# Performance work log

Hardware: AMD Instinct MI355X
Metric: run time of the kernel (lower is better)

Reference implementation:

```python
import jax, jax.numpy as jnp
import numpy as np

EMBED_DIM = 512
N_HEADS = 8
HEAD_DIM = EMBED_DIM // N_HEADS


def setup_inputs() -> dict:
    key = jax.random.key(0)
    ks = jax.random.split(key, 8)
    B, S, D = 8, 2048, EMBED_DIM
    scale = 1.0 / np.sqrt(D)
    return {
        "key": jax.random.normal(ks[0], (B, S, D), dtype=jnp.float32),
        "query": jax.random.normal(ks[1], (B, S, D), dtype=jnp.float32),
        "value": jax.random.normal(ks[2], (B, S, D), dtype=jnp.float32),
        # nn.Linear stores weight as [out, in]; y = x @ W.T. We store W_T=[in,out].
        "Wq": jax.random.normal(ks[3], (D, D), dtype=jnp.float32) * scale,
        "Wk": jax.random.normal(ks[4], (D, D), dtype=jnp.float32) * scale,
        "Wv": jax.random.normal(ks[5], (D, D), dtype=jnp.float32) * scale,
        "Wo": jax.random.normal(ks[6], (D, D), dtype=jnp.float32) * scale,
        "bo": jax.random.normal(ks[7], (D,), dtype=jnp.float32) * scale,
    }


def reference(key, query, value, Wq, Wk, Wv, Wo, bo):
    B, S, D = key.shape
    Sq = query.shape[1]
    H, Hd = N_HEADS, HEAD_DIM
    # projections (no bias for q/k/v)
    q = (query @ Wq).reshape(B, Sq, H, Hd)
    k = (key @ Wk).reshape(B, S, H, Hd)
    v = (value @ Wv).reshape(B, S, H, Hd)
    # scores: [B, H, Sq, S]
    product = jnp.einsum("bqhd,bkhd->bhqk", q, k) / np.sqrt(Hd)
    scores = jax.nn.softmax(product, axis=-1)
    out = jnp.einsum("bhqk,bkhd->bqhd", scores, v).reshape(B, Sq, D)
    return out @ Wo + bo
```

## Files before the change

### kernel.cpp

```cpp
#include <hip/hip_runtime.h>

typedef _Float16 half8 __attribute__((ext_vector_type(8)));
typedef _Float16 half4 __attribute__((ext_vector_type(4)));
typedef float floatx16 __attribute__((ext_vector_type(16)));

#define MFMA_F16 __builtin_amdgcn_mfma_f32_32x32x16_f16

__device__ __forceinline__ half8 ld_frag_lds(const _Float16* p) {
    union { half8 v; half4 h[2]; } u;
    u.h[0] = *(const half4*)(p);
    u.h[1] = *(const half4*)(p + 4);
    return u.v;
}

__global__ __launch_bounds__(256) void wcvt_kernel(const float* __restrict__ Wq,
                                                   const float* __restrict__ Wk,
                                                   const float* __restrict__ Wv,
                                                   const float* __restrict__ Wo,
                                                   _Float16* __restrict__ Wt) {
    int idx = blockIdx.x * 256 + threadIdx.x;
    int wsel = idx >> 18;
    int rem  = idx & 262143;
    int o = rem >> 9;
    int i = rem & 511;
    const float* src = (wsel == 0) ? Wq : (wsel == 1) ? Wk : (wsel == 2) ? Wv : Wo;
    Wt[idx] = (_Float16)src[i * 512 + o];
}

template <int MODE>
__global__ __launch_bounds__(256, 3) void gemm_kernel(const void* __restrict__ Aptr,
                                                      const _Float16* __restrict__ Wt,
                                                      const float* __restrict__ bias,
                                                      void* __restrict__ outp,
                                                      float oscale) {
    __shared__ _Float16 Alds[128 * 68];
    __shared__ _Float16 Blds[128 * 68];

    const int tid  = threadIdx.x;
    const int lane = tid & 63;
    const int w    = tid >> 6;
    const int l31  = lane & 31;
    const int lh   = lane >> 5;
    const int wm   = w >> 1;
    const int wn   = w & 1;
    const int n0   = blockIdx.x * 128;
    const int m0   = blockIdx.y * 128;

    const int crow = tid >> 3;
    const int ck8  = (tid & 7) * 8;

    floatx16 acc[2][2];
#pragma unroll
    for (int i = 0; i < 2; i++)
#pragma unroll
        for (int j = 0; j < 2; j++)
#pragma unroll
            for (int r = 0; r < 16; r++) acc[i][j][r] = 0.0f;

    float4 apre_f[4][2];
    int4   apre_h[4];
    if (MODE == 2) {
        const _Float16* Ah = (const _Float16*)Aptr;
#pragma unroll
        for (int i = 0; i < 4; i++)
            apre_h[i] = *(const int4*)(Ah + (size_t)(m0 + crow + 32 * i) * 512 + ck8);
    } else {
        const float* Af = (const float*)Aptr;
#pragma unroll
        for (int i = 0; i < 4; i++) {
            const float* p = Af + (size_t)(m0 + crow + 32 * i) * 512 + ck8;
            apre_f[i][0] = *(const float4*)(p);
            apre_f[i][1] = *(const float4*)(p + 4);
        }
    }

    for (int t = 0; t < 8; t++) {
        const int ks = t * 64;
        int4 bpre[4];
#pragma unroll
        for (int i = 0; i < 4; i++)
            bpre[i] = *(const int4*)(Wt + (size_t)(n0 + crow + 32 * i) * 512 + ks + ck8);

        __syncthreads();
#pragma unroll
        for (int i = 0; i < 4; i++) {
            int r = crow + 32 * i;
            if (MODE == 2) {
                *(int2*)&Alds[r * 68 + ck8]     = make_int2(apre_h[i].x, apre_h[i].y);
                *(int2*)&Alds[r * 68 + ck8 + 4] = make_int2(apre_h[i].z, apre_h[i].w);
            } else {
                float4 f0 = apre_f[i][0], f1 = apre_f[i][1];
                half4 h0 = {(_Float16)f0.x, (_Float16)f0.y, (_Float16)f0.z, (_Float16)f0.w};
                half4 h1 = {(_Float16)f1.x, (_Float16)f1.y, (_Float16)f1.z, (_Float16)f1.w};
                *(half4*)&Alds[r * 68 + ck8]     = h0;
                *(half4*)&Alds[r * 68 + ck8 + 4] = h1;
            }
            *(int2*)&Blds[r * 68 + ck8]     = make_int2(bpre[i].x, bpre[i].y);
            *(int2*)&Blds[r * 68 + ck8 + 4] = make_int2(bpre[i].z, bpre[i].w);
        }
        __syncthreads();

        if (t < 7) {
            if (MODE == 2) {
                const _Float16* Ah = (const _Float16*)Aptr;
#pragma unroll
                for (int i = 0; i < 4; i++)
                    apre_h[i] = *(const int4*)(Ah + (size_t)(m0 + crow + 32 * i) * 512 + ks + 64 + ck8);
            } else {
                const float* Af = (const float*)Aptr;
#pragma unroll
                for (int i = 0; i < 4; i++) {
                    const float* p = Af + (size_t)(m0 + crow + 32 * i) * 512 + ks + 64 + ck8;
                    apre_f[i][0] = *(const float4*)(p);
                    apre_f[i][1] = *(const float4*)(p + 4);
                }
            }
        }

#pragma unroll
        for (int kc = 0; kc < 4; kc++) {
            int kb = kc * 16 + lh * 8;
            half8 af[2], bf[2];
            af[0] = ld_frag_lds(&Alds[(wm * 64 + l31) * 68 + kb]);
            af[1] = ld_frag_lds(&Alds[(wm * 64 + 32 + l31) * 68 + kb]);
            bf[0] = ld_frag_lds(&Blds[(wn * 64 + l31) * 68 + kb]);
            bf[1] = ld_frag_lds(&Blds[(wn * 64 + 32 + l31) * 68 + kb]);
#pragma unroll
            for (int i = 0; i < 2; i++)
#pragma unroll
                for (int j = 0; j < 2; j++)
                    acc[i][j] = MFMA_F16(af[i], bf[j], acc[i][j], 0, 0, 0);
        }
    }

#pragma unroll
    for (int i = 0; i < 2; i++) {
#pragma unroll
        for (int j = 0; j < 2; j++) {
            int gn    = n0 + wn * 64 + j * 32 + l31;
            int mbase = m0 + wm * 64 + i * 32 + 4 * lh;
            if (MODE == 0) {
                _Float16* out = (_Float16*)outp;
                int h = gn >> 6, hd = gn & 63;
#pragma unroll
                for (int r = 0; r < 16; r++) {
                    int gm = mbase + (r & 3) + 8 * (r >> 2);
                    int b = gm >> 11, s = gm & 2047;
                    out[(size_t)((b * 8 + h) * 2048 + s) * 64 + hd] =
                        (_Float16)(acc[i][j][r] * oscale);
                }
            } else if (MODE == 1) {
                _Float16* out = (_Float16*)outp;
                int h = gn >> 6, hd = gn & 63;
#pragma unroll
                for (int g = 0; g < 4; g++) {
                    int gm = mbase + 8 * g;
                    int b = gm >> 11, s = gm & 2047;
                    half4 pk = {(_Float16)acc[i][j][4 * g + 0], (_Float16)acc[i][j][4 * g + 1],
                                (_Float16)acc[i][j][4 * g + 2], (_Float16)acc[i][j][4 * g + 3]};
                    *(half4*)&out[(size_t)((b * 8 + h) * 64 + hd) * 2048 + s] = pk;
                }
            } else {
                float* out = (float*)outp;
                float bv = bias[gn];
#pragma unroll
                for (int r = 0; r < 16; r++) {
                    int gm = mbase + (r & 3) + 8 * (r >> 2);
                    out[(size_t)gm * 512 + gn] = acc[i][j][r] + bv;
                }
            }
        }
    }
}

__global__ __launch_bounds__(256, 4) void attn_kernel(const _Float16* __restrict__ Qg,
                                                      const _Float16* __restrict__ Kg,
                                                      const _Float16* __restrict__ Vg,
                                                      _Float16* __restrict__ AO) {
    __shared__ _Float16 Klds[64 * 68];
    __shared__ _Float16 Vlds[64 * 68];
    __shared__ _Float16 Plds[4][32 * 68];

    const int tid  = threadIdx.x;
    const int lane = tid & 63;
    const int w    = tid >> 6;
    const int l31  = lane & 31;
    const int lh   = lane >> 5;
    const int h    = blockIdx.y;
    const int b    = blockIdx.z;
    const int q0   = blockIdx.x * 128 + w * 32;

    const size_t bhoff = (size_t)(b * 8 + h) * (2048 * 64);
    const _Float16* Qbh = Qg + bhoff;
    const _Float16* Kbh = Kg + bhoff;
    const _Float16* Vbh = Vg + bhoff;

    half8 qf[4];
#pragma unroll
    for (int kc = 0; kc < 4; kc++)
        qf[kc] = *(const half8*)(Qbh + (size_t)(q0 + l31) * 64 + kc * 16 + lh * 8);

    floatx16 O[2];
#pragma unroll
    for (int i = 0; i < 2; i++)
#pragma unroll
        for (int r = 0; r < 16; r++) O[i][r] = 0.0f;
    float lsum = 0.0f;

    for (int kt = 0; kt < 32; kt++) {
        __syncthreads();
        {
            const _Float16* Ksrc = Kbh + (size_t)kt * (64 * 64);
            const _Float16* Vsrc = Vbh + (size_t)kt * 64;
#pragma unroll
            for (int i = 0; i < 2; i++) {
                int c = tid + 256 * i;
                int row = c >> 3, k8 = (c & 7) * 8;
                int4 dk = *(const int4*)(Ksrc + row * 64 + k8);
                *(int2*)&Klds[row * 68 + k8]     = make_int2(dk.x, dk.y);
                *(int2*)&Klds[row * 68 + k8 + 4] = make_int2(dk.z, dk.w);
                int4 dv = *(const int4*)(Vsrc + (size_t)row * 2048 + k8);
                *(int2*)&Vlds[row * 68 + k8]     = make_int2(dv.x, dv.y);
                *(int2*)&Vlds[row * 68 + k8 + 4] = make_int2(dv.z, dv.w);
            }
        }
        __syncthreads();

        floatx16 Sf[2];
#pragma unroll
        for (int i = 0; i < 2; i++)
#pragma unroll
            for (int r = 0; r < 16; r++) Sf[i][r] = 0.0f;
#pragma unroll
        for (int ms = 0; ms < 2; ms++)
#pragma unroll
            for (int kc = 0; kc < 4; kc++) {
                half8 kf = ld_frag_lds(&Klds[(ms * 32 + l31) * 68 + kc * 16 + lh * 8]);
                Sf[ms] = MFMA_F16(kf, qf[kc], Sf[ms], 0, 0, 0);
            }

        float rsum = 0.0f;
#pragma unroll
        for (int ms = 0; ms < 2; ms++) {
#pragma unroll
            for (int g = 0; g < 4; g++) {
                float p0 = exp2f(Sf[ms][4 * g + 0]);
                float p1 = exp2f(Sf[ms][4 * g + 1]);
                float p2 = exp2f(Sf[ms][4 * g + 2]);
                float p3 = exp2f(Sf[ms][4 * g + 3]);
                rsum += (p0 + p1) + (p2 + p3);
                half4 pk = {(_Float16)p0, (_Float16)p1, (_Float16)p2, (_Float16)p3};
                *(half4*)&Plds[w][l31 * 68 + ms * 32 + g * 8 + lh * 4] = pk;
            }
        }
        lsum += rsum;

#pragma unroll
        for (int kc = 0; kc < 4; kc++) {
            half8 pf = ld_frag_lds(&Plds[w][l31 * 68 + kc * 16 + lh * 8]);
#pragma unroll
            for (int hs = 0; hs < 2; hs++) {
                half8 vf = ld_frag_lds(&Vlds[(hs * 32 + l31) * 68 + kc * 16 + lh * 8]);
                O[hs] = MFMA_F16(vf, pf, O[hs], 0, 0, 0);
            }
        }
    }

    lsum += __shfl_xor(lsum, 32);
    float inv = 1.0f / lsum;
    int q = q0 + l31;
#pragma unroll
    for (int hs = 0; hs < 2; hs++) {
#pragma unroll
        for (int g = 0; g < 4; g++) {
            half4 pk = {(_Float16)(O[hs][4 * g + 0] * inv),
                        (_Float16)(O[hs][4 * g + 1] * inv),
                        (_Float16)(O[hs][4 * g + 2] * inv),
                        (_Float16)(O[hs][4 * g + 3] * inv)};
            *(half4*)&AO[(size_t)(b * 2048 + q) * 512 + h * 64 + hs * 32 + g * 8 + lh * 4] = pk;
        }
    }
}

extern "C" void kernel_launch(void* const* d_in, const int* in_sizes, int n_in,
                              void* d_out, int out_size, void* d_ws, size_t ws_size,
                              hipStream_t stream) {
    const float* key   = (const float*)d_in[0];
    const float* query = (const float*)d_in[1];
    const float* value = (const float*)d_in[2];
    const float* Wq    = (const float*)d_in[3];
    const float* Wk    = (const float*)d_in[4];
    const float* Wv    = (const float*)d_in[5];
    const float* Wo    = (const float*)d_in[6];
    const float* bo    = (const float*)d_in[7];

    _Float16* ws = (_Float16*)d_ws;
    _Float16* Wt = ws;
    _Float16* Qh = ws + 1048576;
    _Float16* Kh = Qh + 8388608;
    _Float16* Vt = Kh + 8388608;
    _Float16* AO = Vt + 8388608;

    const float C1 = 0.18033688011112042f;

    wcvt_kernel<<<dim3(4096), dim3(256), 0, stream>>>(Wq, Wk, Wv, Wo, Wt);

    gemm_kernel<0><<<dim3(4, 128), dim3(256), 0, stream>>>(query, Wt,            nullptr, Qh, C1);
    gemm_kernel<0><<<dim3(4, 128), dim3(256), 0, stream>>>(key,   Wt + 262144,   nullptr, Kh, 1.0f);
    gemm_kernel<1><<<dim3(4, 128), dim3(256), 0, stream>>>(value, Wt + 2*262144, nullptr, Vt, 1.0f);

    attn_kernel<<<dim3(16, 8, 8), dim3(256), 0, stream>>>(Qh, Kh, Vt, AO);

    gemm_kernel<2><<<dim3(4, 128), dim3(256), 0, stream>>>(AO, Wt + 3*262144, bo, (float*)d_out, 1.0f);
}
```

Measured before the change: 334.5 us.

## Merge QKV GEMMs, prefetch K/V tiles in attention, tile weight transpose

Merges the three projection GEMM launches into one 3D grid, which removes launch gaps and leaves the GPU less idle at kernel tails. The weight conversion becomes an LDS-tiled transpose, so global reads and writes are coalesced. The attention kernel now register-prefetches the next K/V tile so the global loads overlap the MFMA work, and the GEMM B loads are double-buffered the same way. It also uses a hardware exp2 and packed round-toward-zero fp16 conversions, which raise register pressure and change rounding slightly.

Measured after the change: 298.1 us. -10.9%, faster.

```diff
diff --git a/kernel.cpp b/kernel.cpp
--- a/kernel.cpp
+++ b/kernel.cpp
@@ -2,9 +2,25 @@
 
 typedef _Float16 half8 __attribute__((ext_vector_type(8)));
 typedef _Float16 half4 __attribute__((ext_vector_type(4)));
+typedef __fp16 fp16x2 __attribute__((ext_vector_type(2)));
 typedef float floatx16 __attribute__((ext_vector_type(16)));
 
 #define MFMA_F16 __builtin_amdgcn_mfma_f32_32x32x16_f16
+
+__device__ __forceinline__ float fast_exp2(float x) {
+#if __has_builtin(__builtin_amdgcn_exp2f)
+    return __builtin_amdgcn_exp2f(x);
+#else
+    return exp2f(x);
+#endif
+}
+
+__device__ __forceinline__ half4 pack4(float a, float b, float c, float d) {
+    union { fp16x2 p[2]; half4 h; } u;
+    u.p[0] = __builtin_amdgcn_cvt_pkrtz(a, b);
+    u.p[1] = __builtin_amdgcn_cvt_pkrtz(c, d);
+    return u.h;
+}
 
 __device__ __forceinline__ half8 ld_frag_lds(const _Float16* p) {
     union { half8 v; half4 h[2]; } u;
@@ -18,23 +34,52 @@
                                                    const float* __restrict__ Wv,
                                                    const float* __restrict__ Wo,
                                                    _Float16* __restrict__ Wt) {
-    int idx = blockIdx.x * 256 + threadIdx.x;
-    int wsel = idx >> 18;
-    int rem  = idx & 262143;
-    int o = rem >> 9;
-    int i = rem & 511;
+    __shared__ _Float16 T[64 * 68];
+    const int bx   = blockIdx.x;
+    const int wsel = bx >> 6;
+    const int tile = bx & 63;
+    const int to   = (tile >> 3) * 64;
+    const int ti   = (tile & 7) * 64;
     const float* src = (wsel == 0) ? Wq : (wsel == 1) ? Wk : (wsel == 2) ? Wv : Wo;
-    Wt[idx] = (_Float16)src[i * 512 + o];
-}
-
-template <int MODE>
-__global__ __launch_bounds__(256, 3) void gemm_kernel(const void* __restrict__ Aptr,
-                                                      const _Float16* __restrict__ Wt,
-                                                      const float* __restrict__ bias,
-                                                      void* __restrict__ outp,
-                                                      float oscale) {
+    const int t = threadIdx.x;
+    const int rloc = t >> 4, c4 = (t & 15) * 4;
+#pragma unroll
+    for (int m = 0; m < 4; m++) {
+        int i = ti + rloc + 16 * m;
+        float4 f = *(const float4*)(src + (size_t)i * 512 + to + c4);
+        T[(c4 + 0) * 68 + rloc + 16 * m] = (_Float16)f.x;
+        T[(c4 + 1) * 68 + rloc + 16 * m] = (_Float16)f.y;
+        T[(c4 + 2) * 68 + rloc + 16 * m] = (_Float16)f.z;
+        T[(c4 + 3) * 68 + rloc + 16 * m] = (_Float16)f.w;
+    }
+    __syncthreads();
+    const int o_loc = t >> 2, ich = (t & 3) * 16;
+    const _Float16* s = &T[o_loc * 68 + ich];
+    _Float16* dst = Wt + (size_t)wsel * 262144 + (size_t)(to + o_loc) * 512 + ti + ich;
+    half4 a0 = *(const half4*)(s);
+    half4 a1 = *(const half4*)(s + 4);
+    half4 a2 = *(const half4*)(s + 8);
+    half4 a3 = *(const half4*)(s + 12);
+    *(half4*)(dst)      = a0;
+    *(half4*)(dst + 4)  = a1;
+    *(half4*)(dst + 8)  = a2;
+    *(half4*)(dst + 12) = a3;
+}
+
+__global__ __launch_bounds__(256, 3) void qkv_gemm(const float* __restrict__ query,
+                                                   const float* __restrict__ key,
+                                                   const float* __restrict__ value,
+                                                   const _Float16* __restrict__ Wt,
+                                                   _Float16* __restrict__ Qh,
+                                                   _Float16* __restrict__ Kh,
+                                                   _Float16* __restrict__ Vt,
+                                                   float C1) {
     __shared__ _Float16 Alds[128 * 68];
     __shared__ _Float16 Blds[128 * 68];
+
+    const int z = blockIdx.z;
+    const float* A = (z == 0) ? query : (z == 1) ? key : value;
+    const _Float16* W = Wt + (size_t)z * 262144;
 
     const int tid  = threadIdx.x;
     const int lane = tid & 63;
@@ -45,7 +90,6 @@
     const int wn   = w & 1;
     const int n0   = blockIdx.x * 128;
     const int m0   = blockIdx.y * 128;
-
     const int crow = tid >> 3;
     const int ck8  = (tid & 7) * 8;
 
@@ -57,66 +101,38 @@
 #pragma unroll
             for (int r = 0; r < 16; r++) acc[i][j][r] = 0.0f;
 
-    float4 apre_f[4][2];
-    int4   apre_h[4];
-    if (MODE == 2) {
-        const _Float16* Ah = (const _Float16*)Aptr;
-#pragma unroll
-        for (int i = 0; i < 4; i++)
-            apre_h[i] = *(const int4*)(Ah + (size_t)(m0 + crow + 32 * i) * 512 + ck8);
-    } else {
-        const float* Af = (const float*)Aptr;
-#pragma unroll
-        for (int i = 0; i < 4; i++) {
-            const float* p = Af + (size_t)(m0 + crow + 32 * i) * 512 + ck8;
-            apre_f[i][0] = *(const float4*)(p);
-            apre_f[i][1] = *(const float4*)(p + 4);
-        }
+    float4 apre[4][2];
+    int4   bpre[4];
+#pragma unroll
+    for (int i = 0; i < 4; i++) {
+        const float* p = A + (size_t)(m0 + crow + 32 * i) * 512 + ck8;
+        apre[i][0] = *(const float4*)(p);
+        apre[i][1] = *(const float4*)(p + 4);
+        bpre[i] = *(const int4*)(W + (size_t)(n0 + crow + 32 * i) * 512 + ck8);
     }
 
     for (int t = 0; t < 8; t++) {
-        const int ks = t * 64;
-        int4 bpre[4];
-#pragma unroll
-        for (int i = 0; i < 4; i++)
-            bpre[i] = *(const int4*)(Wt + (size_t)(n0 + crow + 32 * i) * 512 + ks + ck8);
-
         __syncthreads();
 #pragma unroll
         for (int i = 0; i < 4; i++) {
             int r = crow + 32 * i;
-            if (MODE == 2) {
-                *(int2*)&Alds[r * 68 + ck8]     = make_int2(apre_h[i].x, apre_h[i].y);
-                *(int2*)&Alds[r * 68 + ck8 + 4] = make_int2(apre_h[i].z, apre_h[i].w);
-            } else {
-                float4 f0 = apre_f[i][0], f1 = apre_f[i][1];
-                half4 h0 = {(_Float16)f0.x, (_Float16)f0.y, (_Float16)f0.z, (_Float16)f0.w};
-                half4 h1 = {(_Float16)f1.x, (_Float16)f1.y, (_Float16)f1.z, (_Float16)f1.w};
-                *(half4*)&Alds[r * 68 + ck8]     = h0;
-                *(half4*)&Alds[r * 68 + ck8 + 4] = h1;
-            }
-            *(int2*)&Blds[r * 68 + ck8]     = make_int2(bpre[i].x, bpre[i].y);
-            *(int2*)&Blds[r * 68 + ck8 + 4] = make_int2(bpre[i].z, bpre[i].w);
-        }
-        __syncthreads();
-
+            float4 f0 = apre[i][0], f1 = apre[i][1];
+            *(half4*)&Alds[r * 68 + ck8]     = pack4(f0.x, f0.y, f0.z, f0.w);
+            *(half4*)&Alds[r * 68 + ck8 + 4] = pack4(f1.x, f1.y, f1.z, f1.w);
+            *(int2*)&Blds[r * 68 + ck8]      = make_int2(bpre[i].x, bpre[i].y);
+            *(int2*)&Blds[r * 68 + ck8 + 4]  = make_int2(bpre[i].z, bpre[i].w);
+        }
+        __syncthreads();
         if (t < 7) {
-            if (MODE == 2) {
-                const _Float16* Ah = (const _Float16*)Aptr;
-#pragma unroll
-                for (int i = 0; i < 4; i++)
-                    apre_h[i] = *(const int4*)(Ah + (size_t)(m0 + crow + 32 * i) * 512 + ks + 64 + ck8);
-            } else {
-                const float* Af = (const float*)Aptr;
-#pragma unroll
-                for (int i = 0; i < 4; i++) {
-                    const float* p = Af + (size_t)(m0 + crow + 32 * i) * 512 + ks + 64 + ck8;
-                    apre_f[i][0] = *(const float4*)(p);
-                    apre_f[i][1] = *(const float4*)(p + 4);
-                }
-            }
-        }
-
+            int ks2 = (t + 1) * 64;
+#pragma unroll
+            for (int i = 0; i < 4; i++) {
+                const float* p = A + (size_t)(m0 + crow + 32 * i) * 512 + ks2 + ck8;
+                apre[i][0] = *(const float4*)(p);
+                apre[i][1] = *(const float4*)(p + 4);
+                bpre[i] = *(const int4*)(W + (size_t)(n0 + crow + 32 * i) * 512 + ks2 + ck8);
+            }
+        }
 #pragma unroll
         for (int kc = 0; kc < 4; kc++) {
             int kb = kc * 16 + lh * 8;
@@ -133,41 +149,117 @@
         }
     }
 
+    const float oscale = (z == 0) ? C1 : 1.0f;
+    _Float16* out01 = (z == 0) ? Qh : Kh;
 #pragma unroll
     for (int i = 0; i < 2; i++) {
 #pragma unroll
         for (int j = 0; j < 2; j++) {
             int gn    = n0 + wn * 64 + j * 32 + l31;
             int mbase = m0 + wm * 64 + i * 32 + 4 * lh;
-            if (MODE == 0) {
-                _Float16* out = (_Float16*)outp;
-                int h = gn >> 6, hd = gn & 63;
+            int h = gn >> 6, hd = gn & 63;
+            if (z < 2) {
 #pragma unroll
                 for (int r = 0; r < 16; r++) {
                     int gm = mbase + (r & 3) + 8 * (r >> 2);
                     int b = gm >> 11, s = gm & 2047;
-                    out[(size_t)((b * 8 + h) * 2048 + s) * 64 + hd] =
+                    out01[(size_t)((b * 8 + h) * 2048 + s) * 64 + hd] =
                         (_Float16)(acc[i][j][r] * oscale);
                 }
-            } else if (MODE == 1) {
-                _Float16* out = (_Float16*)outp;
-                int h = gn >> 6, hd = gn & 63;
+            } else {
 #pragma unroll
                 for (int g = 0; g < 4; g++) {
                     int gm = mbase + 8 * g;
                     int b = gm >> 11, s = gm & 2047;
-                    half4 pk = {(_Float16)acc[i][j][4 * g + 0], (_Float16)acc[i][j][4 * g + 1],
-                                (_Float16)acc[i][j][4 * g + 2], (_Float16)acc[i][j][4 * g + 3]};
-                    *(half4*)&out[(size_t)((b * 8 + h) * 64 + hd) * 2048 + s] = pk;
+                    *(half4*)&Vt[(size_t)((b * 8 + h) * 64 + hd) * 2048 + s] =
+                        pack4(acc[i][j][4 * g + 0], acc[i][j][4 * g + 1],
+                              acc[i][j][4 * g + 2], acc[i][j][4 * g + 3]);
                 }
-            } else {
-                float* out = (float*)outp;
-                float bv = bias[gn];
-#pragma unroll
-                for (int r = 0; r < 16; r++) {
-                    int gm = mbase + (r & 3) + 8 * (r >> 2);
-                    out[(size_t)gm * 512 + gn] = acc[i][j][r] + bv;
-                }
+            }
+        }
+    }
+}
+
+__global__ __launch_bounds__(256, 3) void out_gemm(const _Float16* __restrict__ A,
+                                                   const _Float16* __restrict__ W,
+                                                   const float* __restrict__ bias,
+                                                   float* __restrict__ out) {
+    __shared__ _Float16 Alds[128 * 68];
+    __shared__ _Float16 Blds[128 * 68];
+
+    const int tid  = threadIdx.x;
+    const int lane = tid & 63;
+    const int w    = tid >> 6;
+    const int l31  = lane & 31;
+    const int lh   = lane >> 5;
+    const int wm   = w >> 1;
+    const int wn   = w & 1;
+    const int n0   = blockIdx.x * 128;
+    const int m0   = blockIdx.y * 128;
+    const int crow = tid >> 3;
+    const int ck8  = (tid & 7) * 8;
+
+    floatx16 acc[2][2];
+#pragma unroll
+    for (int i = 0; i < 2; i++)
+#pragma unroll
+        for (int j = 0; j < 2; j++)
+#pragma unroll
+            for (int r = 0; r < 16; r++) acc[i][j][r] = 0.0f;
+
+    int4 apre[4], bpre[4];
+#pragma unroll
+    for (int i = 0; i < 4; i++) {
+        apre[i] = *(const int4*)(A + (size_t)(m0 + crow + 32 * i) * 512 + ck8);
+        bpre[i] = *(const int4*)(W + (size_t)(n0 + crow + 32 * i) * 512 + ck8);
+    }
+
+    for (int t = 0; t < 8; t++) {
+        __syncthreads();
+#pragma unroll
+        for (int i = 0; i < 4; i++) {
+            int r = crow + 32 * i;
+            *(int2*)&Alds[r * 68 + ck8]     = make_int2(apre[i].x, apre[i].y);
+            *(int2*)&Alds[r * 68 + ck8 + 4] = make_int2(apre[i].z, apre[i].w);
+            *(int2*)&Blds[r * 68 + ck8]     = make_int2(bpre[i].x, bpre[i].y);
+            *(int2*)&Blds[r * 68 + ck8 + 4] = make_int2(bpre[i].z, bpre[i].w);
+        }
+        __syncthreads();
+        if (t < 7) {
+            int ks2 = (t + 1) * 64;
+#pragma unroll
+            for (int i = 0; i < 4; i++) {
+                apre[i] = *(const int4*)(A + (size_t)(m0 + crow + 32 * i) * 512 + ks2 + ck8);
+                bpre[i] = *(const int4*)(W + (size_t)(n0 + crow + 32 * i) * 512 + ks2 + ck8);
+            }
+        }
+#pragma unroll
+        for (int kc = 0; kc < 4; kc++) {
+            int kb = kc * 16 + lh * 8;
+            half8 af[2], bf[2];
+            af[0] = ld_frag_lds(&Alds[(wm * 64 + l31) * 68 + kb]);
+            af[1] = ld_frag_lds(&Alds[(wm * 64 + 32 + l31) * 68 + kb]);
+            bf[0] = ld_frag_lds(&Blds[(wn * 64 + l31) * 68 + kb]);
+            bf[1] = ld_frag_lds(&Blds[(wn * 64 + 32 + l31) * 68 + kb]);
+#pragma unroll
+            for (int i = 0; i < 2; i++)
+#pragma unroll
+                for (int j = 0; j < 2; j++)
+                    acc[i][j] = MFMA_F16(af[i], bf[j], acc[i][j], 0, 0, 0);
+        }
+    }
+
+#pragma unroll
+    for (int i = 0; i < 2; i++) {
+#pragma unroll
+        for (int j = 0; j < 2; j++) {
+            int gn    = n0 + wn * 64 + j * 32 + l31;
+            int mbase = m0 + wm * 64 + i * 32 + 4 * lh;
+            float bv = bias[gn];
+#pragma unroll
+            for (int r = 0; r < 16; r++) {
+                int gm = mbase + (r & 3) + 8 * (r >> 2);
+                out[(size_t)gm * 512 + gn] = acc[i][j][r] + bv;
             }
         }
     }
@@ -195,6 +287,9 @@
     const _Float16* Kbh = Kg + bhoff;
     const _Float16* Vbh = Vg + bhoff;
 
+    const int c0row = tid >> 3, ck8 = (tid & 7) * 8;
+    const int c1row = c0row + 32;
+
     half8 qf[4];
 #pragma unroll
     for (int kc = 0; kc < 4; kc++)
@@ -207,24 +302,32 @@
         for (int r = 0; r < 16; r++) O[i][r] = 0.0f;
     float lsum = 0.0f;
 
+    int4 kpre[2], vpre[2];
+    kpre[0] = *(const int4*)(Kbh + c0row * 64 + ck8);
+    kpre[1] = *(const int4*)(Kbh + c1row * 64 + ck8);
+    vpre[0] = *(const int4*)(Vbh + (size_t)c0row * 2048 + ck8);
+    vpre[1] = *(const int4*)(Vbh + (size_t)c1row * 2048 + ck8);
+
     for (int kt = 0; kt < 32; kt++) {
         __syncthreads();
-        {
-            const _Float16* Ksrc = Kbh + (size_t)kt * (64 * 64);
-            const _Float16* Vsrc = Vbh + (size_t)kt * 64;
-#pragma unroll
-            for (int i = 0; i < 2; i++) {
-                int c = tid + 256 * i;
-                int row = c >> 3, k8 = (c & 7) * 8;
-                int4 dk = *(const int4*)(Ksrc + row * 64 + k8);
-                *(int2*)&Klds[row * 68 + k8]     = make_int2(dk.x, dk.y);
-                *(int2*)&Klds[row * 68 + k8 + 4] = make_int2(dk.z, dk.w);
-                int4 dv = *(const int4*)(Vsrc + (size_t)row * 2048 + k8);
-                *(int2*)&Vlds[row * 68 + k8]     = make_int2(dv.x, dv.y);
-                *(int2*)&Vlds[row * 68 + k8 + 4] = make_int2(dv.z, dv.w);
-            }
-        }
-        __syncthreads();
+        *(int2*)&Klds[c0row * 68 + ck8]     = make_int2(kpre[0].x, kpre[0].y);
+        *(int2*)&Klds[c0row * 68 + ck8 + 4] = make_int2(kpre[0].z, kpre[0].w);
+        *(int2*)&Klds[c1row * 68 + ck8]     = make_int2(kpre[1].x, kpre[1].y);
+        *(int2*)&Klds[c1row * 68 + ck8 + 4] = make_int2(kpre[1].z, kpre[1].w);
+        *(int2*)&Vlds[c0row * 68 + ck8]     = make_int2(vpre[0].x, vpre[0].y);
+        *(int2*)&Vlds[c0row * 68 + ck8 + 4] = make_int2(vpre[0].z, vpre[0].w);
+        *(int2*)&Vlds[c1row * 68 + ck8]     = make_int2(vpre[1].x, vpre[1].y);
+        *(int2*)&Vlds[c1row * 68 + ck8 + 4] = make_int2(vpre[1].z, vpre[1].w);
+        __syncthreads();
+
+        if (kt < 31) {
+            const _Float16* Ksrc = Kbh + (size_t)(kt + 1) * 4096;
+            const _Float16* Vsrc = Vbh + (size_t)(kt + 1) * 64;
+            kpre[0] = *(const int4*)(Ksrc + c0row * 64 + ck8);
+            kpre[1] = *(const int4*)(Ksrc + c1row * 64 + ck8);
+            vpre[0] = *(const int4*)(Vsrc + (size_t)c0row * 2048 + ck8);
+            vpre[1] = *(const int4*)(Vsrc + (size_t)c1row * 2048 + ck8);
+        }
 
         floatx16 Sf[2];
 #pragma unroll
@@ -239,21 +342,22 @@
                 Sf[ms] = MFMA_F16(kf, qf[kc], Sf[ms], 0, 0, 0);
             }
 
-        float rsum = 0.0f;
+        float rsA = 0.0f, rsB = 0.0f;
 #pragma unroll
         for (int ms = 0; ms < 2; ms++) {
 #pragma unroll
             for (int g = 0; g < 4; g++) {
-                float p0 = exp2f(Sf[ms][4 * g + 0]);
-                float p1 = exp2f(Sf[ms][4 * g + 1]);
-                float p2 = exp2f(Sf[ms][4 * g + 2]);
-                float p3 = exp2f(Sf[ms][4 * g + 3]);
-                rsum += (p0 + p1) + (p2 + p3);
-                half4 pk = {(_Float16)p0, (_Float16)p1, (_Float16)p2, (_Float16)p3};
-                *(half4*)&Plds[w][l31 * 68 + ms * 32 + g * 8 + lh * 4] = pk;
-            }
-        }
-        lsum += rsum;
+                float p0 = fast_exp2(Sf[ms][4 * g + 0]);
+                float p1 = fast_exp2(Sf[ms][4 * g + 1]);
+                float p2 = fast_exp2(Sf[ms][4 * g + 2]);
+                float p3 = fast_exp2(Sf[ms][4 * g + 3]);
+                rsA += p0 + p1;
+                rsB += p2 + p3;
+                *(half4*)&Plds[w][l31 * 68 + ms * 32 + g * 8 + lh * 4] =
+                    pack4(p0, p1, p2, p3);
+            }
+        }
+        lsum += rsA + rsB;
 
 #pragma unroll
         for (int kc = 0; kc < 4; kc++) {
@@ -273,11 +377,9 @@
     for (int hs = 0; hs < 2; hs++) {
 #pragma unroll
         for (int g = 0; g < 4; g++) {
-            half4 pk = {(_Float16)(O[hs][4 * g + 0] * inv),
-                        (_Float16)(O[hs][4 * g + 1] * inv),
-                        (_Float16)(O[hs][4 * g + 2] * inv),
-                        (_Float16)(O[hs][4 * g + 3] * inv)};
-            *(half4*)&AO[(size_t)(b * 2048 + q) * 512 + h * 64 + hs * 32 + g * 8 + lh * 4] = pk;
+            *(half4*)&AO[(size_t)(b * 2048 + q) * 512 + h * 64 + hs * 32 + g * 8 + lh * 4] =
+                pack4(O[hs][4 * g + 0] * inv, O[hs][4 * g + 1] * inv,
+                      O[hs][4 * g + 2] * inv, O[hs][4 * g + 3] * inv);
         }
     }
 }
@@ -303,13 +405,13 @@
 
     const float C1 = 0.18033688011112042f;
 
-    wcvt_kernel<<<dim3(4096), dim3(256), 0, stream>>>(Wq, Wk, Wv, Wo, Wt);
-
-    gemm_kernel<0><<<dim3(4, 128), dim3(256), 0, stream>>>(query, Wt,            nullptr, Qh, C1);
-    gemm_kernel<0><<<dim3(4, 128), dim3(256), 0, stream>>>(key,   Wt + 262144,   nullptr, Kh, 1.0f);
-    gemm_kernel<1><<<dim3(4, 128), dim3(256), 0, stream>>>(value, Wt + 2*262144, nullptr, Vt, 1.0f);
+    wcvt_kernel<<<dim3(256), dim3(256), 0, stream>>>(Wq, Wk, Wv, Wo, Wt);
+
+    qkv_gemm<<<dim3(4, 128, 3), dim3(256), 0, stream>>>(query, key, value, Wt,
+                                                        Qh, Kh, Vt, C1);
 
     attn_kernel<<<dim3(16, 8, 8), dim3(256), 0, stream>>>(Qh, Kh, Vt, AO);
 
-    gemm_kernel<2><<<dim3(4, 128), dim3(256), 0, stream>>>(AO, Wt + 3*262144, bo, (float*)d_out, 1.0f);
-}
+    out_gemm<<<dim3(4, 128), dim3(256), 0, stream>>>(AO, Wt + 3 * 262144, bo,
+                                                     (float*)d_out);
+}
```
